# Kernel tuning notes

Hardware: AMD Instinct MI355X
Metric: run time of the kernel (lower is better)

Reference implementation:

```python
import jax, jax.numpy as jnp
import numpy as np

EPS = 1e-5
NUM_GROUPS = 8
NUM_HEADS = 8


def setup_inputs() -> dict:
    key = jax.random.key(0)
    ks = jax.random.split(key, 8)
    b, c, d, h, w = 2, 256, 32, 32, 32
    ctx_len, ctx_dim = 77, 768
    inner = 256  # num_heads * head_dim
    sq = 1.0 / np.sqrt(c)
    sc = 1.0 / np.sqrt(ctx_dim)
    si = 1.0 / np.sqrt(inner)
    return {
        "x": jax.random.normal(ks[0], (b, c, d, h, w), jnp.float32),
        "context": jax.random.normal(ks[1], (b, ctx_len, ctx_dim), jnp.float32),
        "gn_gamma": jnp.ones((c,), jnp.float32),
        "gn_beta": jnp.zeros((c,), jnp.float32),
        "ln_gamma": jnp.ones((ctx_dim,), jnp.float32),
        "ln_beta": jnp.zeros((ctx_dim,), jnp.float32),
        "Wq": jax.random.normal(ks[2], (c, inner), jnp.float32) * sq,
        "Wk": jax.random.normal(ks[3], (ctx_dim, inner), jnp.float32) * sc,
        "Wv": jax.random.normal(ks[4], (ctx_dim, inner), jnp.float32) * sc,
        "Wo": jax.random.normal(ks[5], (inner, c), jnp.float32) * si,
        "bo": jnp.zeros((c,), jnp.float32),
    }


def group_norm(x, gamma, beta):
    # x: [b, c, d, h, w]
    b, c = x.shape[0], x.shape[1]
    xg = x.reshape(b, NUM_GROUPS, -1)  # [b, G, (c/G)*dhw]
    mean = jnp.mean(xg, axis=-1, keepdims=True)
    var = jnp.var(xg, axis=-1, keepdims=True)
    xg = (xg - mean) * jax.lax.rsqrt(var + EPS)
    xg = xg.reshape(x.shape)
    return xg * gamma[None, :, None, None, None] + beta[None, :, None, None, None]


def layer_norm(x, gamma, beta):
    mean = jnp.mean(x, axis=-1, keepdims=True)
    var = jnp.var(x, axis=-1, keepdims=True)
    return (x - mean) * jax.lax.rsqrt(var + EPS) * gamma + beta


def reference(x, context, gn_gamma, gn_beta, ln_gamma, ln_beta, Wq, Wk, Wv, Wo, bo):
    b, c, d, h, w = x.shape
    H = NUM_HEADS
    hd = Wq.shape[1] // H
    scale = hd ** (-0.5)

    x_norm = group_norm(x, gn_gamma, gn_beta)
    ctx_norm = layer_norm(context, ln_gamma, ln_beta)

    q_in = x_norm.reshape(b, c, -1).transpose(0, 2, 1)  # [b, q_len, c]
    q = q_in @ Wq          # [b, q_len, H*hd]
    k = ctx_norm @ Wk      # [b, k_len, H*hd]
    v = ctx_norm @ Wv

    qn = q.shape[1]
    kn = k.shape[1]
    q = q.reshape(b, qn, H, hd).transpose(0, 2, 1, 3)  # [b, H, q, hd]
    k = k.reshape(b, kn, H, hd).transpose(0, 2, 1, 3)
    v = v.reshape(b, kn, H, hd).transpose(0, 2, 1, 3)

    attn = jnp.einsum('bhqd,bhkd->bhqk', q, k) * scale
    attn = jax.nn.softmax(attn, axis=-1)
    out = jnp.einsum('bhqk,bhkd->bhqd', attn, v)       # [b, H, q, hd]

    out = out.transpose(0, 2, 1, 3).reshape(b, qn, H * hd)
    out = out @ Wo + bo  # dropout is identity in eval
    out = out.transpose(0, 2, 1).reshape(b, c, d, h, w)
    return x + out
```

## Files before the change

kernel.cpp:

```cpp
#include <hip/hip_runtime.h>
#include <stdint.h>

typedef unsigned short u16;
typedef unsigned int u32;
typedef _Float16 half8 __attribute__((ext_vector_type(8)));
typedef _Float16 half4 __attribute__((ext_vector_type(4)));
typedef float floatx4 __attribute__((ext_vector_type(4)));

__device__ __forceinline__ void splitf(float a, u16* hi, u16* lo) {
  union { _Float16 h; u16 u; } ch, cl;
  ch.h = (_Float16)a;
  cl.h = (_Float16)(a - (float)ch.h);
  *hi = ch.u; *lo = cl.u;
}

__device__ __forceinline__ u16 cvt16(float a) {
  union { _Float16 h; u16 u; } c;
  c.h = (_Float16)a;
  return c.u;
}

__device__ __forceinline__ int qix(int row, int col) {
  int g = (col >> 3) ^ (row & 7) ^ ((row >> 3) & 7);
  return row * 256 + ((g << 3) | (col & 7));
}

__global__ void prep_all(const float* __restrict__ x, float* __restrict__ stats,
                         const float* __restrict__ ctx, const float* __restrict__ lng,
                         const float* __restrict__ lnb, const float* __restrict__ Wk,
                         const float* __restrict__ Wv,
                         u16* __restrict__ kh, u16* __restrict__ vh,
                         const float* __restrict__ wq, const float* __restrict__ wo,
                         u16* __restrict__ wqt, u16* __restrict__ wot) {
  __shared__ float smem[776];
  int bid = blockIdx.x;
  int t = threadIdx.x;

  if (bid < 2048) {
    int bg = bid >> 7;
    int chunk = bid & 127;
    size_t base = ((size_t)bg << 20) + ((size_t)chunk << 13);
    float4 v[8];
#pragma unroll
    for (int it = 0; it < 8; ++it)
      v[it] = *(const float4*)(x + base + (size_t)it * 1024 + t * 4);
    float s = 0.f, sq = 0.f;
#pragma unroll
    for (int it = 0; it < 8; ++it) {
      s += v[it].x + v[it].y + v[it].z + v[it].w;
      sq += v[it].x * v[it].x + v[it].y * v[it].y + v[it].z * v[it].z + v[it].w * v[it].w;
    }
    for (int d = 32; d; d >>= 1) { s += __shfl_xor(s, d, 64); sq += __shfl_xor(sq, d, 64); }
    float* red = smem;
    int wv = t >> 6, lane = t & 63;
    if (lane == 0) { red[wv] = s; red[4 + wv] = sq; }
    __syncthreads();
    if (t == 0) {
      atomicAdd(&stats[bg * 16], red[0] + red[1] + red[2] + red[3]);
      atomicAdd(&stats[256 + bg * 16], red[4] + red[5] + red[6] + red[7]);
    }
    return;
  }

  if (bid < 2432) {
    int kb = bid - 2048;
    int doV = kb >= 192;
    if (doV) kb -= 192;
    int key = kb % 96;
    int b = kb / 96;
    size_t ko = (size_t)(b * 96 + key) * 256 + t;
    size_t vo = ((size_t)(b * 8 + (t >> 5)) * 32 + (t & 31)) * 96 + key;
    if (key >= 77) {
      if (doV) vh[vo] = 0; else kh[ko] = 0;
      return;
    }
    float* lnv = smem;
    float* red = smem + 768;
    const float* row = ctx + (size_t)(b * 77 + key) * 768;
    float v0 = row[t], v1 = row[t + 256], v2 = row[t + 512];
    float s = v0 + v1 + v2, sq = v0 * v0 + v1 * v1 + v2 * v2;
    for (int d = 32; d; d >>= 1) { s += __shfl_xor(s, d, 64); sq += __shfl_xor(sq, d, 64); }
    int wv = t >> 6, lane = t & 63;
    if (!lane) { red[wv] = s; red[4 + wv] = sq; }
    __syncthreads();
    float S = red[0] + red[1] + red[2] + red[3];
    float SQ = red[4] + red[5] + red[6] + red[7];
    const float invD = 1.0f / 768.0f;
    float mean = S * invD;
    float rstd = rsqrtf(SQ * invD - mean * mean + 1e-5f);
    lnv[t]       = (v0 - mean) * rstd * lng[t]       + lnb[t];
    lnv[t + 256] = (v1 - mean) * rstd * lng[t + 256] + lnb[t + 256];
    lnv[t + 512] = (v2 - mean) * rstd * lng[t + 512] + lnb[t + 512];
    __syncthreads();
    const float* W = doV ? Wv : Wk;
    float a0 = 0.f, a1 = 0.f, a2 = 0.f, a3 = 0.f;
    float a4 = 0.f, a5 = 0.f, a6 = 0.f, a7 = 0.f;
    for (int e = 0; e < 768; e += 8) {
      a0 += lnv[e] * W[(e) * 256 + t];         a1 += lnv[e + 1] * W[(e + 1) * 256 + t];
      a2 += lnv[e + 2] * W[(e + 2) * 256 + t]; a3 += lnv[e + 3] * W[(e + 3) * 256 + t];
      a4 += lnv[e + 4] * W[(e + 4) * 256 + t]; a5 += lnv[e + 5] * W[(e + 5) * 256 + t];
      a6 += lnv[e + 6] * W[(e + 6) * 256 + t]; a7 += lnv[e + 7] * W[(e + 7) * 256 + t];
    }
    float a = ((a0 + a1) + (a2 + a3)) + ((a4 + a5) + (a6 + a7));
    if (doV) vh[vo] = cvt16(a); else kh[ko] = cvt16(a);
    return;
  }

  {
    int pb = bid - 2432;
    int bx = pb & 15, by = (pb >> 4) & 15, bz = pb >> 8;
    float (*tile)[17] = (float(*)[17])smem;
    const float* src = bz ? wo : wq;
    u16* dst = bz ? wot : wqt;
    int r0 = by * 16, c0 = bx * 16;
    int r = t >> 4, c = t & 15;
    tile[r][c] = src[(r0 + r) * 256 + c0 + c];
    __syncthreads();
    dst[(c0 + r) * 256 + r0 + c] = cvt16(tile[c][r]);
  }
}

__global__ __launch_bounds__(256, 2) void fused_qao(
    const float* __restrict__ x,
    const u16* __restrict__ wqt, const u16* __restrict__ wot,
    const u16* __restrict__ kws_hi, const u16* __restrict__ vtw_hi,
    const float* __restrict__ gng, const float* __restrict__ gnb,
    const float* __restrict__ stats,
    const float* __restrict__ bo, float* __restrict__ out) {
  __shared__ u16 qhi[64 * 256];
  __shared__ u16 qlo[64 * 256];
  int t = threadIdx.x, lane = t & 63, wv = t >> 6;
  int ml = lane & 15, quad = lane >> 4;
  int b = blockIdx.x >> 9;
  int s0 = (blockIdx.x & 511) * 64;

  {
    const float invN = 1.0f / 1048576.0f;
    int sc_ = (t & 7) * 8;
#pragma unroll
    for (int p = 0; p < 8; ++p) {
      int c = p * 32 + (t >> 3);
      int bg = b * 8 + (c >> 5);
      float mean = stats[bg * 16] * invN;
      float var = stats[256 + bg * 16] * invN - mean * mean;
      float rstd = rsqrtf(var + 1e-5f);
      float scale = rstd * gng[c];
      float shift = gnb[c] - mean * scale;
      size_t base = (((size_t)(b * 256 + c)) << 15) + s0 + sc_;
      float4 xv0 = *(const float4*)(x + base);
      float4 xv1 = *(const float4*)(x + base + 4);
      float xa[8] = {xv0.x, xv0.y, xv0.z, xv0.w, xv1.x, xv1.y, xv1.z, xv1.w};
#pragma unroll
      for (int e = 0; e < 8; ++e) {
        int o = qix(sc_ + e, c);
        splitf(xa[e] * scale + shift, &qhi[o], &qlo[o]);
      }
    }
  }
  __syncthreads();

  floatx4 acc[4][4];
#pragma unroll
  for (int i = 0; i < 4; ++i)
#pragma unroll
    for (int j = 0; j < 4; ++j) acc[i][j] = (floatx4){0.f, 0.f, 0.f, 0.f};
  for (int k0 = 0; k0 < 256; k0 += 32) {
    half8 ah[4], al[4], bh[4];
#pragma unroll
    for (int j = 0; j < 4; ++j) {
      size_t wo_ = (size_t)(wv * 64 + j * 16 + ml) * 256 + k0 + quad * 8;
      bh[j] = *(const half8*)(wqt + wo_);
    }
#pragma unroll
    for (int i = 0; i < 4; ++i) {
      int idx = qix(i * 16 + ml, k0 + quad * 8);
      ah[i] = *(const half8*)&qhi[idx];
      al[i] = *(const half8*)&qlo[idx];
    }
#pragma unroll
    for (int i = 0; i < 4; ++i)
#pragma unroll
      for (int j = 0; j < 4; ++j) {
        acc[i][j] = __builtin_amdgcn_mfma_f32_16x16x32_f16(al[i], bh[j], acc[i][j], 0, 0, 0);
        acc[i][j] = __builtin_amdgcn_mfma_f32_16x16x32_f16(ah[i], bh[j], acc[i][j], 0, 0, 0);
      }
  }
  __syncthreads();
#pragma unroll
  for (int i = 0; i < 4; ++i)
#pragma unroll
    for (int j = 0; j < 4; ++j)
#pragma unroll
      for (int r = 0; r < 4; ++r) {
        int o = qix(i * 16 + quad * 4 + r, wv * 64 + j * 16 + ml);
        qhi[o] = cvt16(acc[i][j][r]);
      }
  __syncthreads();

  int h0 = (wv >> 1) * 4;
  int r16 = (wv & 1) * 16;
  const float scl = 0.17677669529663687f;
  const floatx4 z = {0.f, 0.f, 0.f, 0.f};
  for (int hh = 0; hh < 4; ++hh) {
    int h = h0 + hh;
    half8 kbh[5];
#pragma unroll
    for (int kt = 0; kt < 5; ++kt) {
      size_t ko = (size_t)(b * 96 + kt * 16 + ml) * 256 + h * 32 + quad * 8;
      kbh[kt] = *(const half8*)(kws_hi + ko);
    }
    half4 vfh[2][5];
#pragma unroll
    for (int db = 0; db < 2; ++db)
#pragma unroll
      for (int kt = 0; kt < 5; ++kt) {
        size_t vo = (size_t)((b * 8 + h) * 32 + db * 16 + ml) * 96 + kt * 16 + quad * 4;
        vfh[db][kt] = *(const half4*)(vtw_hi + vo);
      }
#pragma unroll
    for (int rg = 0; rg < 2; ++rg) {
      int qrow = rg * 32 + r16 + ml;
      half8 qfh = *(const half8*)&qhi[qix(qrow, h * 32 + quad * 8)];
      floatx4 sc[5];
      __builtin_amdgcn_s_setprio(1);
#pragma unroll
      for (int kt = 0; kt < 5; ++kt)
        sc[kt] = __builtin_amdgcn_mfma_f32_16x16x32_f16(kbh[kt], qfh, z, 0, 0, 0);
      __builtin_amdgcn_s_setprio(0);
      float mx = -1e30f;
#pragma unroll
      for (int kt = 0; kt < 5; ++kt) {
        int kbase = kt * 16 + quad * 4;
#pragma unroll
        for (int r = 0; r < 4; ++r) {
          float v = (kbase + r < 77) ? sc[kt][r] * scl : -1e30f;
          sc[kt][r] = v;
          mx = fmaxf(mx, v);
        }
      }
      mx = fmaxf(mx, __shfl_xor(mx, 16, 64));
      mx = fmaxf(mx, __shfl_xor(mx, 32, 64));
      float sm = 0.f;
#pragma unroll
      for (int kt = 0; kt < 5; ++kt)
#pragma unroll
        for (int r = 0; r < 4; ++r) {
          float p = __expf(sc[kt][r] - mx);
          sc[kt][r] = p;
          sm += p;
        }
      sm += __shfl_xor(sm, 16, 64);
      sm += __shfl_xor(sm, 32, 64);
      float inv = 1.0f / sm;
      half4 pb[5];
#pragma unroll
      for (int kt = 0; kt < 5; ++kt) {
        pb[kt][0] = (_Float16)(sc[kt][0] * inv);
        pb[kt][1] = (_Float16)(sc[kt][1] * inv);
        pb[kt][2] = (_Float16)(sc[kt][2] * inv);
        pb[kt][3] = (_Float16)(sc[kt][3] * inv);
      }
      floatx4 o0 = z, o1 = z;
      __builtin_amdgcn_s_setprio(1);
#pragma unroll
      for (int kt = 0; kt < 5; ++kt) {
        o0 = __builtin_amdgcn_mfma_f32_16x16x16f16(vfh[0][kt], pb[kt], o0, 0, 0, 0);
        o1 = __builtin_amdgcn_mfma_f32_16x16x16f16(vfh[1][kt], pb[kt], o1, 0, 0, 0);
      }
      __builtin_amdgcn_s_setprio(0);
#pragma unroll
      for (int r = 0; r < 4; ++r) {
        int o0i = qix(qrow, h * 32 + quad * 4 + r);
        splitf(o0[r], &qhi[o0i], &qlo[o0i]);
        int o1i = qix(qrow, h * 32 + 16 + quad * 4 + r);
        splitf(o1[r], &qhi[o1i], &qlo[o1i]);
      }
    }
  }
  __syncthreads();

#pragma unroll
  for (int i = 0; i < 4; ++i)
#pragma unroll
    for (int j = 0; j < 4; ++j) acc[i][j] = (floatx4){0.f, 0.f, 0.f, 0.f};
  for (int k0 = 0; k0 < 256; k0 += 32) {
    half8 ah[4], al[4], bh[4];
#pragma unroll
    for (int j = 0; j < 4; ++j) {
      size_t wo_ = (size_t)(wv * 64 + j * 16 + ml) * 256 + k0 + quad * 8;
      bh[j] = *(const half8*)(wot + wo_);
    }
#pragma unroll
    for (int i = 0; i < 4; ++i) {
      int idx = qix(i * 16 + ml, k0 + quad * 8);
      ah[i] = *(const half8*)&qhi[idx];
      al[i] = *(const half8*)&qlo[idx];
    }
#pragma unroll
    for (int i = 0; i < 4; ++i)
#pragma unroll
      for (int j = 0; j < 4; ++j) {
        acc[i][j] = __builtin_amdgcn_mfma_f32_16x16x32_f16(al[i], bh[j], acc[i][j], 0, 0, 0);
        acc[i][j] = __builtin_amdgcn_mfma_f32_16x16x32_f16(ah[i], bh[j], acc[i][j], 0, 0, 0);
      }
  }
#pragma unroll
  for (int i = 0; i < 4; ++i) {
    int sp = s0 + i * 16 + quad * 4;
#pragma unroll
    for (int j = 0; j < 4; ++j) {
      int col = wv * 64 + j * 16 + ml;
      float bias = bo[col];
      size_t o = (((size_t)(b * 256 + col)) << 15) + sp;
      float4 xv = *(const float4*)(x + o);
      float4 ov;
      ov.x = acc[i][j][0] + bias + xv.x;
      ov.y = acc[i][j][1] + bias + xv.y;
      ov.z = acc[i][j][2] + bias + xv.z;
      ov.w = acc[i][j][3] + bias + xv.w;
      *(float4*)(out + o) = ov;
    }
  }
}

extern "C" void kernel_launch(void* const* d_in, const int* in_sizes, int n_in,
                              void* d_out, int out_size, void* d_ws, size_t ws_size,
                              hipStream_t stream) {
  (void)out_size; (void)ws_size;
  int idx[11] = {0, 1, 2, 3, 4, 5, 6, 7, 8, 9, 10};
  static const int dsz[11] = {16777216, 118272, 256, 256, 768, 768,
                              65536, 196608, 196608, 65536, 256};
  bool dict = (n_in == 11);
  if (dict)
    for (int i = 0; i < 11; ++i)
      if (in_sizes[i] != dsz[i]) { dict = false; break; }
  if (!dict && n_in == 11) {
    static const int ssz[11] = {196608, 65536, 65536, 196608, 256, 118272,
                                256, 256, 768, 768, 16777216};
    bool srt = true;
    for (int i = 0; i < 11; ++i)
      if (in_sizes[i] != ssz[i]) { srt = false; break; }
    if (srt) {
      idx[0] = 10; idx[1] = 5; idx[2] = 7; idx[3] = 6; idx[4] = 9; idx[5] = 8;
      idx[6] = 2;  idx[7] = 0; idx[8] = 3; idx[9] = 1; idx[10] = 4;
    }
  }
  const float* x   = (const float*)d_in[idx[0]];
  const float* ctx = (const float*)d_in[idx[1]];
  const float* gng = (const float*)d_in[idx[2]];
  const float* gnb = (const float*)d_in[idx[3]];
  const float* lng = (const float*)d_in[idx[4]];
  const float* lnb = (const float*)d_in[idx[5]];
  const float* Wq  = (const float*)d_in[idx[6]];
  const float* Wk  = (const float*)d_in[idx[7]];
  const float* Wv  = (const float*)d_in[idx[8]];
  const float* Wo  = (const float*)d_in[idx[9]];
  const float* bo  = (const float*)d_in[idx[10]];
  float* out = (float*)d_out;

  u16* ws = (u16*)d_ws;
  float* stats = (float*)ws;
  u16* wqt    = ws + 1024;
  u16* wot    = wqt + 65536;
  u16* kws_hi = wot + 65536;
  u16* vtw_hi = kws_hi + 49152;

  hipMemsetAsync(stats, 0, 512 * sizeof(float), stream);
  prep_all<<<2944, 256, 0, stream>>>(x, stats, ctx, lng, lnb, Wk, Wv,
                                     kws_hi, vtw_hi,
                                     Wq, Wo, wqt, wot);
  fused_qao<<<1024, 256, 0, stream>>>(x, wqt, wot, kws_hi, vtw_hi,
                                      gng, gnb, stats, bo, out);
}
```

Before: 222.5 us.

## Drop fp16 hi/lo split, raise occupancy, replace atomic stats with per-chunk partials

Removes the hi/lo fp16 error-compensation split for the activation operand in both projection GEMMs and the attention output, halving MFMA count and the LDS footprint. With the lo buffer gone, launch bounds go from 2 to 4 blocks per CU. Group-norm statistics are now stored as per-chunk partials instead of atomics, which removes the memset; each fused block reduces those partials itself. This costs accuracy, since activations become plain fp16, and adds a small reduction at the start of each block.

```diff
diff --git a/kernel.cpp b/kernel.cpp
--- a/kernel.cpp
+++ b/kernel.cpp
@@ -6,13 +6,6 @@
 typedef _Float16 half8 __attribute__((ext_vector_type(8)));
 typedef _Float16 half4 __attribute__((ext_vector_type(4)));
 typedef float floatx4 __attribute__((ext_vector_type(4)));
-
-__device__ __forceinline__ void splitf(float a, u16* hi, u16* lo) {
-  union { _Float16 h; u16 u; } ch, cl;
-  ch.h = (_Float16)a;
-  cl.h = (_Float16)(a - (float)ch.h);
-  *hi = ch.u; *lo = cl.u;
-}
 
 __device__ __forceinline__ u16 cvt16(float a) {
   union { _Float16 h; u16 u; } c;
@@ -56,8 +49,8 @@
     if (lane == 0) { red[wv] = s; red[4 + wv] = sq; }
     __syncthreads();
     if (t == 0) {
-      atomicAdd(&stats[bg * 16], red[0] + red[1] + red[2] + red[3]);
-      atomicAdd(&stats[256 + bg * 16], red[4] + red[5] + red[6] + red[7]);
+      stats[bg * 128 + chunk] = red[0] + red[1] + red[2] + red[3];
+      stats[2048 + bg * 128 + chunk] = red[4] + red[5] + red[6] + red[7];
     }
     return;
   }
@@ -120,7 +113,7 @@
   }
 }
 
-__global__ __launch_bounds__(256, 2) void fused_qao(
+__global__ __launch_bounds__(256, 4) void fused_qao(
     const float* __restrict__ x,
     const u16* __restrict__ wqt, const u16* __restrict__ wot,
     const u16* __restrict__ kws_hi, const u16* __restrict__ vtw_hi,
@@ -128,21 +121,32 @@
     const float* __restrict__ stats,
     const float* __restrict__ bo, float* __restrict__ out) {
   __shared__ u16 qhi[64 * 256];
-  __shared__ u16 qlo[64 * 256];
+  __shared__ float st[16];
   int t = threadIdx.x, lane = t & 63, wv = t >> 6;
   int ml = lane & 15, quad = lane >> 4;
   int b = blockIdx.x >> 9;
   int s0 = (blockIdx.x & 511) * 64;
 
+#pragma unroll
+  for (int gi = 0; gi < 2; ++gi) {
+    int g = wv * 2 + gi;
+    int bg = b * 8 + g;
+    float s = stats[bg * 128 + lane] + stats[bg * 128 + 64 + lane];
+    float sq = stats[2048 + bg * 128 + lane] + stats[2048 + bg * 128 + 64 + lane];
+    for (int d = 32; d; d >>= 1) { s += __shfl_xor(s, d, 64); sq += __shfl_xor(sq, d, 64); }
+    if (lane == 0) { st[g * 2] = s; st[g * 2 + 1] = sq; }
+  }
+  __syncthreads();
+
   {
     const float invN = 1.0f / 1048576.0f;
     int sc_ = (t & 7) * 8;
 #pragma unroll
     for (int p = 0; p < 8; ++p) {
       int c = p * 32 + (t >> 3);
-      int bg = b * 8 + (c >> 5);
-      float mean = stats[bg * 16] * invN;
-      float var = stats[256 + bg * 16] * invN - mean * mean;
+      int g = c >> 5;
+      float mean = st[g * 2] * invN;
+      float var = st[g * 2 + 1] * invN - mean * mean;
       float rstd = rsqrtf(var + 1e-5f);
       float scale = rstd * gng[c];
       float shift = gnb[c] - mean * scale;
@@ -151,10 +155,8 @@
       float4 xv1 = *(const float4*)(x + base + 4);
       float xa[8] = {xv0.x, xv0.y, xv0.z, xv0.w, xv1.x, xv1.y, xv1.z, xv1.w};
 #pragma unroll
-      for (int e = 0; e < 8; ++e) {
-        int o = qix(sc_ + e, c);
-        splitf(xa[e] * scale + shift, &qhi[o], &qlo[o]);
-      }
+      for (int e = 0; e < 8; ++e)
+        qhi[qix(sc_ + e, c)] = cvt16(xa[e] * scale + shift);
     }
   }
   __syncthreads();
@@ -165,25 +167,20 @@
 #pragma unroll
     for (int j = 0; j < 4; ++j) acc[i][j] = (floatx4){0.f, 0.f, 0.f, 0.f};
   for (int k0 = 0; k0 < 256; k0 += 32) {
-    half8 ah[4], al[4], bh[4];
+    half8 ah[4], bh[4];
 #pragma unroll
     for (int j = 0; j < 4; ++j) {
       size_t wo_ = (size_t)(wv * 64 + j * 16 + ml) * 256 + k0 + quad * 8;
       bh[j] = *(const half8*)(wqt + wo_);
     }
 #pragma unroll
-    for (int i = 0; i < 4; ++i) {
-      int idx = qix(i * 16 + ml, k0 + quad * 8);
-      ah[i] = *(const half8*)&qhi[idx];
-      al[i] = *(const half8*)&qlo[idx];
-    }
-#pragma unroll
     for (int i = 0; i < 4; ++i)
-#pragma unroll
-      for (int j = 0; j < 4; ++j) {
-        acc[i][j] = __builtin_amdgcn_mfma_f32_16x16x32_f16(al[i], bh[j], acc[i][j], 0, 0, 0);
+      ah[i] = *(const half8*)&qhi[qix(i * 16 + ml, k0 + quad * 8)];
+#pragma unroll
+    for (int i = 0; i < 4; ++i)
+#pragma unroll
+      for (int j = 0; j < 4; ++j)
         acc[i][j] = __builtin_amdgcn_mfma_f32_16x16x32_f16(ah[i], bh[j], acc[i][j], 0, 0, 0);
-      }
   }
   __syncthreads();
 #pragma unroll
@@ -270,10 +267,8 @@
       __builtin_amdgcn_s_setprio(0);
 #pragma unroll
       for (int r = 0; r < 4; ++r) {
-        int o0i = qix(qrow, h * 32 + quad * 4 + r);
-        splitf(o0[r], &qhi[o0i], &qlo[o0i]);
-        int o1i = qix(qrow, h * 32 + 16 + quad * 4 + r);
-        splitf(o1[r], &qhi[o1i], &qlo[o1i]);
+        qhi[qix(qrow, h * 32 + quad * 4 + r)] = cvt16(o0[r]);
+        qhi[qix(qrow, h * 32 + 16 + quad * 4 + r)] = cvt16(o1[r]);
       }
     }
   }
@@ -284,25 +279,20 @@
 #pragma unroll
     for (int j = 0; j < 4; ++j) acc[i][j] = (floatx4){0.f, 0.f, 0.f, 0.f};
   for (int k0 = 0; k0 < 256; k0 += 32) {
-    half8 ah[4], al[4], bh[4];
+    half8 ah[4], bh[4];
 #pragma unroll
     for (int j = 0; j < 4; ++j) {
       size_t wo_ = (size_t)(wv * 64 + j * 16 + ml) * 256 + k0 + quad * 8;
       bh[j] = *(const half8*)(wot + wo_);
     }
 #pragma unroll
-    for (int i = 0; i < 4; ++i) {
-      int idx = qix(i * 16 + ml, k0 + quad * 8);
-      ah[i] = *(const half8*)&qhi[idx];
-      al[i] = *(const half8*)&qlo[idx];
-    }
-#pragma unroll
     for (int i = 0; i < 4; ++i)
-#pragma unroll
-      for (int j = 0; j < 4; ++j) {
-        acc[i][j] = __builtin_amdgcn_mfma_f32_16x16x32_f16(al[i], bh[j], acc[i][j], 0, 0, 0);
+      ah[i] = *(const half8*)&qhi[qix(i * 16 + ml, k0 + quad * 8)];
+#pragma unroll
+    for (int i = 0; i < 4; ++i)
+#pragma unroll
+      for (int j = 0; j < 4; ++j)
         acc[i][j] = __builtin_amdgcn_mfma_f32_16x16x32_f16(ah[i], bh[j], acc[i][j], 0, 0, 0);
-      }
   }
 #pragma unroll
   for (int i = 0; i < 4; ++i) {
@@ -360,12 +350,11 @@
 
   u16* ws = (u16*)d_ws;
   float* stats = (float*)ws;
-  u16* wqt    = ws + 1024;
+  u16* wqt    = ws + 8192;
   u16* wot    = wqt + 65536;
   u16* kws_hi = wot + 65536;
   u16* vtw_hi = kws_hi + 49152;
 
-  hipMemsetAsync(stats, 0, 512 * sizeof(float), stream);
   prep_all<<<2944, 256, 0, stream>>>(x, stats, ctx, lng, lnb, Wk, Wv,
                                      kws_hi, vtw_hi,
                                      Wq, Wo, wqt, wot);
```

Result: slower. 239.9 us (+7.8%).
